# Performance work log

Hardware: AMD Instinct MI355X
Metric: run time of the kernel (lower is better)

## Reference

```python
import jax, jax.numpy as jnp
import numpy as np

TAU = 2.0        # LIFNode tau
ALPHA = 4.0      # spikingjelly default Sigmoid surrogate alpha
SCALE = 0.125    # attention scale from SSA
EPS = 1e-5       # BatchNorm eps

@jax.custom_vjp
def heaviside(x):
    return (x >= 0).astype(x.dtype)

def _hv_fwd(x):
    return (x >= 0).astype(x.dtype), x

def _hv_bwd(x, g):
    s = jax.nn.sigmoid(ALPHA * x)
    return (g * ALPHA * s * (1.0 - s),)

heaviside.defvjp(_hv_fwd, _hv_bwd)

def lif(x_seq, v_th):
    """Multi-step LIF (decay_input=True, v_reset=0, hard reset, detach_reset=True).
    x_seq: (T, ...) -> spikes (T, ...)."""
    def step(v, x):
        h = v + (x - v) / TAU                      # membrane charge
        s = heaviside(h - v_th)                    # spike
        v_new = h * (1.0 - jax.lax.stop_gradient(s))  # detached hard reset to 0
        return v_new, s
    _, spikes = jax.lax.scan(step, jnp.zeros_like(x_seq[0]), x_seq)
    return spikes

def conv_bn(x, w, gamma, beta, mean, var):
    """3x3 same-pad conv (no bias) + BatchNorm2d (eval: running stats), applied over merged T*B."""
    T, B, C, H, W = x.shape
    y = jax.lax.conv_general_dilated(
        x.reshape(T * B, C, H, W), w, (1, 1), 'SAME',
        dimension_numbers=('NCHW', 'OIHW', 'NCHW'))
    scale = gamma / jnp.sqrt(var + EPS)
    y = y * scale[:, None, None] + (beta - mean * scale)[:, None, None]
    return y.reshape(T, B, C, H, W)

def setup_inputs() -> dict:
    key = jax.random.key(0)
    T, B, C, H, W = 4, 16, 768, 16, 16
    ks = jax.random.split(key, 5)
    d = {"x": jax.random.normal(ks[0], (T, B, C, H, W), jnp.float32)}
    for i, p in enumerate(["q", "k", "v", "p"]):
        kk = jax.random.split(ks[i + 1], 5)
        d[p + "_w"] = jax.random.normal(kk[0], (C, C, 3, 3), jnp.float32) * 0.02
        d[p + "_gamma"] = jax.random.uniform(kk[1], (C,), jnp.float32, 0.5, 1.5)
        d[p + "_beta"] = jax.random.normal(kk[2], (C,), jnp.float32) * 0.1
        d[p + "_mean"] = jax.random.normal(kk[3], (C,), jnp.float32) * 0.1
        d[p + "_var"] = jax.random.uniform(kk[4], (C,), jnp.float32, 0.5, 1.5)
    return d

def reference(x, q_w, q_gamma, q_beta, q_mean, q_var,
              k_w, k_gamma, k_beta, k_mean, k_var,
              v_w, v_gamma, v_beta, v_mean, v_var,
              p_w, p_gamma, p_beta, p_mean, p_var):
    T, B, C, H, W = x.shape
    N = H * W
    nh = 8
    dh = C // nh
    xs = lif(x, 1.0)                                   # head_lif
    # Scaler is identity in eval mode (and rate=1.0)
    q = lif(conv_bn(xs, q_w, q_gamma, q_beta, q_mean, q_var), 1.0)
    k = lif(conv_bn(xs, k_w, k_gamma, k_beta, k_mean, k_var), 1.0)
    v = lif(conv_bn(xs, v_w, v_gamma, v_beta, v_mean, v_var), 1.0)
    def to_heads(t):  # (T,B,C,H,W) -> (T,B,nh,N,dh)
        return t.reshape(T, B, C, N).transpose(0, 1, 3, 2).reshape(T, B, N, nh, dh).transpose(0, 1, 3, 2, 4)
    q, k, v = to_heads(q), to_heads(k), to_heads(v)
    kv = jnp.einsum('tbhnd,tbhne->tbhde', k, v)        # k^T @ v (linear attention)
    o = jnp.einsum('tbhnd,tbhde->tbhne', q, kv) * SCALE
    o = o.transpose(0, 1, 2, 4, 3).reshape(T, B, C, N)  # (T,B,h,d,N) -> (T,B,C,N)
    o = lif(o, 0.5).reshape(T, B, C, H, W)              # attn_lif with v_threshold=0.5
    return conv_bn(o, p_w, p_gamma, p_beta, p_mean, p_var)
```

## Files before the change

kernel.cpp:

```cpp
#include <hip/hip_runtime.h>

typedef __attribute__((ext_vector_type(4))) int   i32x4;
typedef __attribute__((ext_vector_type(4))) float f32x4;
typedef unsigned int u32;
typedef unsigned long long u64;
typedef unsigned char u8;
typedef unsigned short u16;

#define C_ 768
#define NPIX 256
#define PLANE (16*C_*NPIX)
#define ROWB 96
#define IMGBITS (324*ROWB)
#define GS   304
#define PRS  1232
#define AEXP_SZ 12320

#define OFF_WFRAG 0ull
#define OFF_YBUF  10616832ull
#define OFF_QU8   60948480ull
#define OFF_KU8   73531392ull
#define OFF_VU8   86114304ull
#define OFF_OU8   98697216ull
#define OFF_BITS  111280128ull
#define BITSZ     1990656ull
#define OFF_SBT   121233408ull
#define OFF_FLAGS 121257984ull
#define OFF_WMAX  121258240ull

__device__ __forceinline__ i32x4 as_i4(uint4 v){ union{uint4 u; i32x4 s;} c; c.u=v; return c.s; }
#define SPREAD(NIB) ((u32)__mul24((int)(NIB), 0x204081) & 0x01010101u)

__global__ __launch_bounds__(256) void bn_prep4(
    const float* __restrict__ g0, const float* __restrict__ b0,
    const float* __restrict__ m0, const float* __restrict__ v0,
    const float* __restrict__ g1, const float* __restrict__ b1,
    const float* __restrict__ m1, const float* __restrict__ v1,
    const float* __restrict__ g2, const float* __restrict__ b2,
    const float* __restrict__ m2, const float* __restrict__ v2,
    const float* __restrict__ g3, const float* __restrict__ b3,
    const float* __restrict__ m3, const float* __restrict__ v3,
    float* __restrict__ out)
{
    int s = blockIdx.y;
    const float* g  = s==0?g0:s==1?g1:s==2?g2:g3;
    const float* be = s==0?b0:s==1?b1:s==2?b2:b3;
    const float* m  = s==0?m0:s==1?m1:s==2?m2:m3;
    const float* va = s==0?v0:s==1?v1:s==2?v2:v3;
    int i = blockIdx.x*256 + threadIdx.x;
    if (i < C_){
        float sc = g[i] / sqrtf(va[i] + 1e-5f);
        out[s*1536 + i] = sc;
        out[s*1536 + C_ + i] = be[i] - m[i]*sc;
    }
}

__global__ __launch_bounds__(256) void wmax4(
    const float* __restrict__ w0, const float* __restrict__ w1,
    const float* __restrict__ w2, const float* __restrict__ w3,
    float* __restrict__ out)
{
    int s = blockIdx.y;
    const float* w = s==0?w0:s==1?w1:s==2?w2:w3;
    const int n4 = 9*C_*C_/4;
    float m = 0.f;
    for (int i = blockIdx.x*256 + threadIdx.x; i < n4; i += 65536){
        f32x4 v = *(const f32x4*)(w + (size_t)i*4);
        m = fmaxf(m, fmaxf(fmaxf(fabsf(v[0]), fabsf(v[1])),
                           fmaxf(fabsf(v[2]), fabsf(v[3]))));
    }
    #pragma unroll
    for (int off = 32; off >= 1; off >>= 1)
        m = fmaxf(m, __shfl_xor(m, off));
    if ((threadIdx.x & 63) == 0)
        atomicMax((int*)(out + s), __float_as_int(m));
}

__global__ __launch_bounds__(256) void wprep(
    const float* __restrict__ w, const float* __restrict__ wmaxp,
    u8* __restrict__ wf)
{
    int gid = blockIdx.x*256 + threadIdx.x;
    int co = gid / 48, c16 = gid - co*48;
    float mw = *wmaxp;
    float invS = (mw > 0.f) ? (32512.0f / mw) : 0.f;
    int cch = c16 >> 2;
    int lane = (co & 15) | ((c16 & 3) << 4);
    int nfg = co >> 4;
    const float* wp = w + (size_t)co*6912 + (size_t)c16*144;
    #pragma unroll 1
    for (int tap=0; tap<9; ++tap){
        u32 hw[4] = {0,0,0,0}, lw[4] = {0,0,0,0};
        #pragma unroll
        for (int e=0;e<16;++e){
            float f = wp[e*9 + tap];
            int w16 = __float2int_rn(f * invS);
            w16 = min(max(w16, -32512), 32512);
            int hi = (w16 + 128) >> 8;
            int lo = w16 - (hi << 8);
            hw[e>>2] |= ((u32)(hi & 0xFF)) << ((e&3)*8);
            lw[e>>2] |= ((u32)(lo & 0xFF)) << ((e&3)*8);
        }
        size_t base = (((size_t)(cch*9+tap)*48 + nfg)*2)*1024 + (size_t)lane*16;
        *(uint4*)(wf + base)        = make_uint4(hw[0],hw[1],hw[2],hw[3]);
        *(uint4*)(wf + base + 1024) = make_uint4(lw[0],lw[1],lw[2],lw[3]);
    }
}

__global__ __launch_bounds__(256) void head_bits(
    const float* __restrict__ x, u8* __restrict__ bits)
{
    int gid = blockIdx.x*256 + threadIdx.x;
    int b = gid / 24576, rem = gid - b*24576;
    int cb = rem >> 8, pix = rem & 255;
    int pr = ((pix>>4)+1)*18 + (pix&15) + 1;
    float v[8];
    #pragma unroll
    for (int j=0;j<8;++j) v[j]=0.f;
    #pragma unroll
    for (int t=0;t<4;++t){
        int img = t*16 + b;
        u32 byte = 0;
        #pragma unroll
        for (int j=0;j<8;++j){
            float xv = x[((size_t)img*C_ + cb*8 + j)*NPIX + pix];
            float h = __fadd_rn(v[j], __fmul_rn(__fsub_rn(xv, v[j]), 0.5f));
            u32 s = (h >= 1.0f) ? 1u : 0u;
            v[j] = s ? 0.f : h;
            byte |= s << j;
        }
        bits[(size_t)img*IMGBITS + (size_t)pr*ROWB + cb] = (u8)byte;
    }
}

template<int EPI>
__global__ __launch_bounds__(256,2) void conv_i8(
    const u8* __restrict__ abits, const u8* __restrict__ wf,
    const float* __restrict__ sb, const float* __restrict__ wmaxp,
    const int* __restrict__ flags,
    float* __restrict__ ybuf, float* __restrict__ out)
{
    __shared__ __align__(16) u8 Aexp[2*AEXP_SZ];
    const int tid = threadIdx.x;
    const int bid = blockIdx.x;
    const int cox = bid & 7, mh = (bid >> 3) & 1, img = bid >> 4;
    const int lane = tid & 63, w = tid >> 6;
    const int wr = w >> 1, wc = w & 1;
    const int lrow = lane & 15, lgrp = lane >> 4;

    if constexpr (EPI == 1){
        if (flags[img] == 0){
            #pragma unroll 1
            for (int i = tid; i < 96*32; i += 256){
                int co = cox*96 + (i >> 5), seg = i & 31;
                float bv = sb[C_ + co];
                f32x4 v; v[0]=bv; v[1]=bv; v[2]=bv; v[3]=bv;
                *(f32x4*)(out + ((size_t)img*C_ + co)*NPIX + mh*128 + seg*4) = v;
            }
            return;
        }
    }

    const int erow = (tid < 180) ? tid : 179;
    const int epr = erow / 18, epc = erow - epr*18;
    u8* edst = Aexp + epr*PRS + epc*16;
    const u8* bsrc = abits + (size_t)img*IMGBITS + (size_t)(mh*144)*ROWB;

#define EXPW(BW, BOFF) if (tid < 180){ \
    u8* dp = edst + (BOFF); \
    u32 lo_ = (u32)(BW), hi_ = (u32)((BW)>>32); \
    *(uint4*)(dp       ) = make_uint4(SPREAD(lo_&0xF), SPREAD((lo_>>4)&0xF), SPREAD((lo_>>8)&0xF), SPREAD((lo_>>12)&0xF)); \
    *(uint4*)(dp + GS  ) = make_uint4(SPREAD((lo_>>16)&0xF), SPREAD((lo_>>20)&0xF), SPREAD((lo_>>24)&0xF), SPREAD((lo_>>28)&0xF)); \
    *(uint4*)(dp + 2*GS) = make_uint4(SPREAD(hi_&0xF), SPREAD((hi_>>4)&0xF), SPREAD((hi_>>8)&0xF), SPREAD((hi_>>12)&0xF)); \
    *(uint4*)(dp + 3*GS) = make_uint4(SPREAD((hi_>>16)&0xF), SPREAD((hi_>>20)&0xF), SPREAD((hi_>>24)&0xF), SPREAD((hi_>>28)&0xF)); }

    const u8* wp = wf + (size_t)((cox*6 + wc*3)*2)*1024 + (size_t)lane*16;
    uint4 R0[6], R1[6], R2[6];
#define LOADB(BUF) { \
    _Pragma("unroll") \
    for (int j=0;j<6;++j) BUF[j] = *(const uint4*)(wp + (j>>1)*2048 + (j&1)*1024); \
    wp += 98304; }

    int rb[4];
    #pragma unroll
    for (int mi=0;mi<4;++mi)
        rb[mi] = (wr*4 + mi + 1)*PRS + lgrp*GS + (lrow+1)*16;

    i32x4 acc_h[4][3], acc_l[4][3];
    #pragma unroll
    for (int mi=0;mi<4;++mi)
        #pragma unroll
        for (int ni=0;ni<3;++ni)
            #pragma unroll
            for (int r=0;r<4;++r){ acc_h[mi][ni][r]=0; acc_l[mi][ni][r]=0; }

#define COMPUTE(BUF, AE, TAP) { \
    const int DT = ((TAP)/3 - 1)*PRS + (((TAP)%3) - 1)*16; \
    i32x4 af[4]; \
    _Pragma("unroll") \
    for (int mi=0;mi<4;++mi) af[mi] = *(const i32x4*)((AE) + rb[mi] + DT); \
    __builtin_amdgcn_s_setprio(1); \
    _Pragma("unroll") \
    for (int mi=0;mi<4;++mi){ \
        _Pragma("unroll") \
        for (int ni=0;ni<3;++ni){ \
            acc_h[mi][ni] = __builtin_amdgcn_mfma_i32_16x16x64_i8(af[mi], as_i4(BUF[ni*2+0]), acc_h[mi][ni], 0,0,0); \
            acc_l[mi][ni] = __builtin_amdgcn_mfma_i32_16x16x64_i8(af[mi], as_i4(BUF[ni*2+1]), acc_l[mi][ni], 0,0,0); \
        } \
    } \
    __builtin_amdgcn_s_setprio(0); }

#define BODY(CCH, BOFF) { \
    u64 bwn = 0; \
    if ((CCH) < 11) bwn = *(const u64*)(bsrc + erow*ROWB + ((CCH)+1)*8); \
    const u8* Ae = Aexp + (BOFF); \
    LOADB(R2); COMPUTE(R0, Ae, 0); \
    LOADB(R0); COMPUTE(R1, Ae, 1); \
    LOADB(R1); COMPUTE(R2, Ae, 2); \
    LOADB(R2); COMPUTE(R0, Ae, 3); \
    LOADB(R0); COMPUTE(R1, Ae, 4); \
    LOADB(R1); COMPUTE(R2, Ae, 5); \
    LOADB(R2); COMPUTE(R0, Ae, 6); \
    LOADB(R0); COMPUTE(R1, Ae, 7); \
    LOADB(R1); COMPUTE(R2, Ae, 8); \
    if ((CCH) < 11) EXPW(bwn, (BOFF) ^ AEXP_SZ); \
    __syncthreads(); }

    LOADB(R0); LOADB(R1);
    {
        u64 bw0 = *(const u64*)(bsrc + erow*ROWB);
        EXPW(bw0, 0);
    }
    __syncthreads();

    #pragma unroll 1
    for (int c2=0; c2<6; ++c2){
        BODY(2*c2,   0);
        BODY(2*c2+1, AEXP_SZ);
    }
#undef LOADB
#undef EXPW
#undef COMPUTE
#undef BODY

    const float S = (*wmaxp) * (1.0f/32512.0f);
    #pragma unroll
    for (int mi=0;mi<4;++mi){
        const int prow = mh*128 + wr*64 + mi*16 + lgrp*4;
        #pragma unroll
        for (int ni=0;ni<3;++ni){
            const int co = cox*96 + wc*48 + ni*16 + lrow;
            const float sc = sb[co], bi = sb[C_ + co];
            if constexpr (EPI == 0){
                #pragma unroll
                for (int r=0;r<4;++r){
                    float accf = (float)(acc_h[mi][ni][r]*256 + acc_l[mi][ni][r]) * S;
                    ybuf[((size_t)img*NPIX + prow + r)*C_ + co] =
                        __fadd_rn(__fmul_rn(accf, sc), bi);
                }
            } else {
                f32x4 ov;
                #pragma unroll
                for (int r=0;r<4;++r){
                    float accf = (float)(acc_h[mi][ni][r]*256 + acc_l[mi][ni][r]) * S;
                    ov[r] = __fadd_rn(__fmul_rn(accf, sc), bi);
                }
                *(f32x4*)(out + ((size_t)img*C_ + co)*NPIX + prow) = ov;
            }
        }
    }
}

__global__ __launch_bounds__(256) void lif_bits(
    const float* __restrict__ y, u8* __restrict__ su8, u8* __restrict__ bits)
{
    int gid = blockIdx.x*256 + threadIdx.x;
    int b = gid / 24576, rem = gid - b*24576;
    int pix = rem / 96, cb = rem - pix*96;
    int pr = ((pix>>4)+1)*18 + (pix&15) + 1;
    float v[8];
    #pragma unroll
    for (int j=0;j<8;++j) v[j]=0.f;
    #pragma unroll
    for (int t=0;t<4;++t){
        int img = t*16 + b;
        const float* yp = y + ((size_t)img*NPIX + pix)*C_ + cb*8;
        f32x4 y0 = *(const f32x4*)yp;
        f32x4 y1 = *(const f32x4*)(yp + 4);
        u32 byte = 0, w0 = 0, w1 = 0;
        #pragma unroll
        for (int j=0;j<8;++j){
            float yv = (j<4) ? y0[j] : y1[j-4];
            float h = __fadd_rn(v[j], __fmul_rn(__fsub_rn(yv, v[j]), 0.5f));
            u32 s = (h >= 1.0f) ? 1u : 0u;
            v[j] = s ? 0.f : h;
            byte |= s << j;
            if (j<4) w0 |= s << (j*8); else w1 |= s << ((j-4)*8);
        }
        *(uint2*)(su8 + ((size_t)img*NPIX + pix)*C_ + cb*8) = make_uint2(w0,w1);
        bits[(size_t)img*IMGBITS + (size_t)pr*ROWB + cb] = (u8)byte;
    }
}

__global__ __launch_bounds__(256) void pad_o_bits(
    const u8* __restrict__ o, u8* __restrict__ bits, int* __restrict__ flags)
{
    int gid = blockIdx.x*256 + threadIdx.x;
    int img = gid / 24576, rem = gid - img*24576;
    int pix = rem / 96, cb = rem - pix*96;
    int pr = ((pix>>4)+1)*18 + (pix&15) + 1;
    uint2 r = *(const uint2*)(o + ((size_t)img*NPIX + pix)*C_ + cb*8);
    u32 byte = 0;
    #pragma unroll
    for (int j=0;j<4;++j){
        byte |= ((r.x >> (j*8)) & 1u) << j;
        byte |= ((r.y >> (j*8)) & 1u) << (j+4);
    }
    bits[(size_t)img*IMGBITS + (size_t)pr*ROWB + cb] = (u8)byte;
    if (__any((int)(r.x | r.y)) && (threadIdx.x & 63) == 0)
        atomicOr(&flags[img], 1);
}

__global__ __launch_bounds__(512) void attn_fused(
    const u8* __restrict__ qs, const u8* __restrict__ ks,
    const u8* __restrict__ vs, u8* __restrict__ os)
{
    const int tid = threadIdx.x;
    const int b = blockIdx.x, h = blockIdx.y;
    __shared__ u64 kb[96][4], vb[96][4];
    __shared__ float kvl[96][96];
    const int w = tid >> 6, lane = tid & 63;
    const int ng = w & 3, n_build = ng*64 + lane;
    const int n = tid & 255, eh = tid >> 8;
    float vmem[48];
    #pragma unroll
    for (int e=0;e<48;++e) vmem[e]=0.f;

    for (int t=0;t<4;++t){
        const int img = t*16 + b;
        const size_t rbase = ((size_t)img*NPIX)*C_ + (size_t)h*96;
        {
            const u8* src = (w < 4 ? ks : vs) + rbase + (size_t)n_build*C_;
            uint4 r[6];
            #pragma unroll
            for (int j=0;j<6;++j) r[j] = ((const uint4*)src)[j];
            u32 wd[24];
            #pragma unroll
            for (int j=0;j<6;++j){ wd[4*j]=r[j].x; wd[4*j+1]=r[j].y; wd[4*j+2]=r[j].z; wd[4*j+3]=r[j].w; }
            u64 (*dst)[4] = (w < 4) ? kb : vb;
            #pragma unroll 1
            for (int d=0; d<96; ++d){
                u32 byte = (wd[d>>2] >> ((d&3)*8)) & 0xFFu;
                u64 m = __ballot((int)byte);
                if (lane == 0) dst[d][ng] = m;
            }
        }
        __syncthreads();
        for (int i = tid; i < 96*96; i += 512){
            int d = i / 96, e = i - d*96;
            int s = 0;
            #pragma unroll
            for (int g=0; g<4; ++g) s += __popcll(kb[d][g] & vb[e][g]);
            kvl[d][e] = (float)s;
        }
        __syncthreads();
        {
            const u8* qsrc = qs + rbase + (size_t)n*C_;
            uint4 r[6];
            #pragma unroll
            for (int j=0;j<6;++j) r[j] = ((const uint4*)qsrc)[j];
            u32 qw[24];
            #pragma unroll
            for (int j=0;j<6;++j){ qw[4*j]=r[j].x; qw[4*j+1]=r[j].y; qw[4*j+2]=r[j].z; qw[4*j+3]=r[j].w; }
            float val[48];
            #pragma unroll
            for (int e=0;e<48;++e) val[e]=0.f;
            #pragma unroll 1
            for (int d=0; d<96; ++d){
                u32 qb = (qw[d>>2] >> ((d&3)*8)) & 0xFFu;
                if (__any((int)qb)){
                    float qf = (float)qb;
                    #pragma unroll
                    for (int e=0;e<48;++e) val[e] += qf * kvl[d][eh*48+e];
                }
            }
            u32 ow[12];
            #pragma unroll
            for (int e=0;e<48;++e){
                float o = val[e]*0.125f;
                float hh = __fadd_rn(vmem[e], __fmul_rn(__fsub_rn(o, vmem[e]), 0.5f));
                u8 s = (hh >= 0.5f) ? 1 : 0;
                vmem[e] = s ? 0.f : hh;
                if ((e&3)==0) ow[e>>2] = (u32)s; else ow[e>>2] |= ((u32)s) << ((e&3)*8);
            }
            uint4* od = (uint4*)(os + rbase + (size_t)n*C_ + eh*48);
            od[0] = make_uint4(ow[0],ow[1],ow[2],ow[3]);
            od[1] = make_uint4(ow[4],ow[5],ow[6],ow[7]);
            od[2] = make_uint4(ow[8],ow[9],ow[10],ow[11]);
        }
        __syncthreads();
    }
}

extern "C" void kernel_launch(void* const* d_in, const int* in_sizes, int n_in,
                              void* d_out, int out_size, void* d_ws, size_t ws_size,
                              hipStream_t stream)
{
    u8* ws = (u8*)d_ws;
    u8* wfrag   = ws + OFF_WFRAG;
    float* ybuf = (float*)(ws + OFF_YBUF);
    u8* q_u8 = ws + OFF_QU8;
    u8* k_u8 = ws + OFF_KU8;
    u8* v_u8 = ws + OFF_VU8;
    u8* o_u8 = ws + OFF_OU8;
    u8* xs_b = ws + OFF_BITS;
    u8* q_b  = ws + OFF_BITS + 1*BITSZ;
    u8* k_b  = ws + OFF_BITS + 2*BITSZ;
    u8* v_b  = ws + OFF_BITS + 3*BITSZ;
    u8* o_b  = ws + OFF_BITS + 4*BITSZ;
    float* sbt = (float*)(ws + OFF_SBT);
    int* flags = (int*)(ws + OFF_FLAGS);
    float* wmaxb = (float*)(ws + OFF_WMAX);
    float* outp = (float*)d_out;

    hipMemsetAsync(ws + OFF_BITS, 0, 5*BITSZ, stream);
    hipMemsetAsync(ws + OFF_FLAGS, 0, 512, stream);

    bn_prep4<<<dim3(3,4),256,0,stream>>>(
        (const float*)d_in[2],  (const float*)d_in[3],  (const float*)d_in[4],  (const float*)d_in[5],
        (const float*)d_in[7],  (const float*)d_in[8],  (const float*)d_in[9],  (const float*)d_in[10],
        (const float*)d_in[12], (const float*)d_in[13], (const float*)d_in[14], (const float*)d_in[15],
        (const float*)d_in[17], (const float*)d_in[18], (const float*)d_in[19], (const float*)d_in[20],
        sbt);
    wmax4<<<dim3(256,4),256,0,stream>>>(
        (const float*)d_in[1], (const float*)d_in[6],
        (const float*)d_in[11], (const float*)d_in[16], wmaxb);
    head_bits<<<1536,256,0,stream>>>((const float*)d_in[0], xs_b);

    u8* u8p[3]  = {q_u8, k_u8, v_u8};
    u8* bitp[3] = {q_b, k_b, v_b};
    for (int s=0;s<3;++s){
        wprep<<<144,256,0,stream>>>((const float*)d_in[1+5*s], wmaxb + s, wfrag);
        conv_i8<0><<<1024,256,0,stream>>>(xs_b, wfrag, sbt + s*1536, wmaxb + s,
                                          nullptr, ybuf, nullptr);
        lif_bits<<<1536,256,0,stream>>>(ybuf, u8p[s], bitp[s]);
    }
    attn_fused<<<dim3(16,8),512,0,stream>>>(q_u8, k_u8, v_u8, o_u8);
    pad_o_bits<<<6144,256,0,stream>>>(o_u8, o_b, flags);
    wprep<<<144,256,0,stream>>>((const float*)d_in[16], wmaxb + 3, wfrag);
    conv_i8<1><<<1024,256,0,stream>>>(o_b, wfrag, sbt + 4608, wmaxb + 3,
                                      flags, nullptr, outp);
}
```

Baseline: 600.7 us.

## Fuse LIF into conv epilogue, sparse bit-driven projection conv, batch weight prep

The q/k/v convolutions now loop over the four timesteps inside one block, carrying the LIF membrane in registers. Each block writes spikes directly, which removes the fp32 ybuf round trip and the separate lif_bits kernel. The attention kernel writes padded bit-packed output directly, and the final projection conv becomes a sparse scatter-add. That scatter-add walks the set spike bits and accumulates int16 column-major weights in shared memory, replacing the dense MFMA conv. Weight prep for all four convs is batched into one launch. The trade-offs are smaller grids (512 blocks) with fewer rows per block, and a projection cost that now depends on spike density.

```diff
diff --git a/kernel.cpp b/kernel.cpp
--- a/kernel.cpp
+++ b/kernel.cpp
@@ -9,24 +9,23 @@
 
 #define C_ 768
 #define NPIX 256
-#define PLANE (16*C_*NPIX)
 #define ROWB 96
 #define IMGBITS (324*ROWB)
-#define GS   304
-#define PRS  1232
-#define AEXP_SZ 12320
-
+#define LGS 288
+#define EPRS 1184
+#define AEXP_SZ 7104
+
+#define WFRAG_SZ 10616832ull
 #define OFF_WFRAG 0ull
-#define OFF_YBUF  10616832ull
-#define OFF_QU8   60948480ull
-#define OFF_KU8   73531392ull
-#define OFF_VU8   86114304ull
-#define OFF_OU8   98697216ull
-#define OFF_BITS  111280128ull
+#define OFF_WCOL  42467328ull
+#define OFF_QU8   53084160ull
+#define OFF_KU8   65667072ull
+#define OFF_VU8   78249984ull
+#define OFF_XSB   90832896ull
+#define OFF_OB    92823552ull
 #define BITSZ     1990656ull
-#define OFF_SBT   121233408ull
-#define OFF_FLAGS 121257984ull
-#define OFF_WMAX  121258240ull
+#define OFF_SBT   94814208ull
+#define OFF_WMAX  94838784ull
 
 __device__ __forceinline__ i32x4 as_i4(uint4 v){ union{uint4 u; i32x4 s;} c; c.u=v; return c.s; }
 #define SPREAD(NIB) ((u32)__mul24((int)(NIB), 0x204081) & 0x01010101u)
@@ -76,13 +75,18 @@
         atomicMax((int*)(out + s), __float_as_int(m));
 }
 
-__global__ __launch_bounds__(256) void wprep(
-    const float* __restrict__ w, const float* __restrict__ wmaxp,
-    u8* __restrict__ wf)
-{
+__global__ __launch_bounds__(256) void wprep4(
+    const float* __restrict__ w0, const float* __restrict__ w1,
+    const float* __restrict__ w2, const float* __restrict__ w3,
+    const float* __restrict__ wmaxb, u8* __restrict__ wfbase,
+    short* __restrict__ wcol)
+{
+    int s = blockIdx.y;
+    const float* w = s==0?w0:s==1?w1:s==2?w2:w3;
+    u8* wf = wfbase + (size_t)s*WFRAG_SZ;
     int gid = blockIdx.x*256 + threadIdx.x;
     int co = gid / 48, c16 = gid - co*48;
-    float mw = *wmaxp;
+    float mw = wmaxb[s];
     float invS = (mw > 0.f) ? (32512.0f / mw) : 0.f;
     int cch = c16 >> 2;
     int lane = (co & 15) | ((c16 & 3) << 4);
@@ -91,11 +95,13 @@
     #pragma unroll 1
     for (int tap=0; tap<9; ++tap){
         u32 hw[4] = {0,0,0,0}, lw[4] = {0,0,0,0};
+        int w16v[16];
         #pragma unroll
         for (int e=0;e<16;++e){
             float f = wp[e*9 + tap];
             int w16 = __float2int_rn(f * invS);
             w16 = min(max(w16, -32512), 32512);
+            w16v[e] = w16;
             int hi = (w16 + 128) >> 8;
             int lo = w16 - (hi << 8);
             hw[e>>2] |= ((u32)(hi & 0xFF)) << ((e&3)*8);
@@ -104,6 +110,11 @@
         size_t base = (((size_t)(cch*9+tap)*48 + nfg)*2)*1024 + (size_t)lane*16;
         *(uint4*)(wf + base)        = make_uint4(hw[0],hw[1],hw[2],hw[3]);
         *(uint4*)(wf + base + 1024) = make_uint4(lw[0],lw[1],lw[2],lw[3]);
+        if (s == 3){
+            #pragma unroll
+            for (int e=0;e<16;++e)
+                wcol[((size_t)tap*C_ + c16*16+e)*C_ + co] = (short)w16v[e];
+        }
     }
 }
 
@@ -133,86 +144,65 @@
     }
 }
 
-template<int EPI>
-__global__ __launch_bounds__(256,2) void conv_i8(
+__global__ __launch_bounds__(256,2) void conv_lif(
     const u8* __restrict__ abits, const u8* __restrict__ wf,
     const float* __restrict__ sb, const float* __restrict__ wmaxp,
-    const int* __restrict__ flags,
-    float* __restrict__ ybuf, float* __restrict__ out)
+    u8* __restrict__ su8)
 {
     __shared__ __align__(16) u8 Aexp[2*AEXP_SZ];
     const int tid = threadIdx.x;
     const int bid = blockIdx.x;
-    const int cox = bid & 7, mh = (bid >> 3) & 1, img = bid >> 4;
+    const int cox = bid & 7, mh = (bid >> 3) & 3, bq = bid >> 5;
     const int lane = tid & 63, w = tid >> 6;
     const int wr = w >> 1, wc = w & 1;
     const int lrow = lane & 15, lgrp = lane >> 4;
 
-    if constexpr (EPI == 1){
-        if (flags[img] == 0){
-            #pragma unroll 1
-            for (int i = tid; i < 96*32; i += 256){
-                int co = cox*96 + (i >> 5), seg = i & 31;
-                float bv = sb[C_ + co];
-                f32x4 v; v[0]=bv; v[1]=bv; v[2]=bv; v[3]=bv;
-                *(f32x4*)(out + ((size_t)img*C_ + co)*NPIX + mh*128 + seg*4) = v;
-            }
-            return;
-        }
-    }
-
-    const int erow = (tid < 180) ? tid : 179;
-    const int epr = erow / 18, epc = erow - epr*18;
-    u8* edst = Aexp + epr*PRS + epc*16;
-    const u8* bsrc = abits + (size_t)img*IMGBITS + (size_t)(mh*144)*ROWB;
-
-#define EXPW(BW, BOFF) if (tid < 180){ \
+    float scs[3], bis[3];
+    #pragma unroll
+    for (int ni=0;ni<3;++ni){
+        int co = cox*96 + wc*48 + ni*16 + lrow;
+        scs[ni] = sb[co]; bis[ni] = sb[C_ + co];
+    }
+    const float S = wmaxp[0] * (1.0f/32512.0f);
+
+    const int rb0 = (wr*2 + 1)*EPRS + lgrp*LGS + (lrow+1)*16;
+    const int rb1 = rb0 + EPRS;
+
+    const int erow = (tid < 108) ? tid : 107;
+    const int epr = erow/18, epc = erow - epr*18;
+    u8* edst = Aexp + epr*EPRS + epc*16;
+
+#define EXPW(BW, BOFF) if (tid < 108){ \
     u8* dp = edst + (BOFF); \
     u32 lo_ = (u32)(BW), hi_ = (u32)((BW)>>32); \
-    *(uint4*)(dp       ) = make_uint4(SPREAD(lo_&0xF), SPREAD((lo_>>4)&0xF), SPREAD((lo_>>8)&0xF), SPREAD((lo_>>12)&0xF)); \
-    *(uint4*)(dp + GS  ) = make_uint4(SPREAD((lo_>>16)&0xF), SPREAD((lo_>>20)&0xF), SPREAD((lo_>>24)&0xF), SPREAD((lo_>>28)&0xF)); \
-    *(uint4*)(dp + 2*GS) = make_uint4(SPREAD(hi_&0xF), SPREAD((hi_>>4)&0xF), SPREAD((hi_>>8)&0xF), SPREAD((hi_>>12)&0xF)); \
-    *(uint4*)(dp + 3*GS) = make_uint4(SPREAD((hi_>>16)&0xF), SPREAD((hi_>>20)&0xF), SPREAD((hi_>>24)&0xF), SPREAD((hi_>>28)&0xF)); }
-
-    const u8* wp = wf + (size_t)((cox*6 + wc*3)*2)*1024 + (size_t)lane*16;
+    *(uint4*)(dp        ) = make_uint4(SPREAD(lo_&0xF), SPREAD((lo_>>4)&0xF), SPREAD((lo_>>8)&0xF), SPREAD((lo_>>12)&0xF)); \
+    *(uint4*)(dp + LGS  ) = make_uint4(SPREAD((lo_>>16)&0xF), SPREAD((lo_>>20)&0xF), SPREAD((lo_>>24)&0xF), SPREAD((lo_>>28)&0xF)); \
+    *(uint4*)(dp + 2*LGS) = make_uint4(SPREAD(hi_&0xF), SPREAD((hi_>>4)&0xF), SPREAD((hi_>>8)&0xF), SPREAD((hi_>>12)&0xF)); \
+    *(uint4*)(dp + 3*LGS) = make_uint4(SPREAD((hi_>>16)&0xF), SPREAD((hi_>>20)&0xF), SPREAD((hi_>>24)&0xF), SPREAD((hi_>>28)&0xF)); }
+
     uint4 R0[6], R1[6], R2[6];
 #define LOADB(BUF) { \
     _Pragma("unroll") \
     for (int j=0;j<6;++j) BUF[j] = *(const uint4*)(wp + (j>>1)*2048 + (j&1)*1024); \
     wp += 98304; }
 
-    int rb[4];
-    #pragma unroll
-    for (int mi=0;mi<4;++mi)
-        rb[mi] = (wr*4 + mi + 1)*PRS + lgrp*GS + (lrow+1)*16;
-
-    i32x4 acc_h[4][3], acc_l[4][3];
-    #pragma unroll
-    for (int mi=0;mi<4;++mi)
-        #pragma unroll
-        for (int ni=0;ni<3;++ni)
-            #pragma unroll
-            for (int r=0;r<4;++r){ acc_h[mi][ni][r]=0; acc_l[mi][ni][r]=0; }
-
 #define COMPUTE(BUF, AE, TAP) { \
-    const int DT = ((TAP)/3 - 1)*PRS + (((TAP)%3) - 1)*16; \
-    i32x4 af[4]; \
-    _Pragma("unroll") \
-    for (int mi=0;mi<4;++mi) af[mi] = *(const i32x4*)((AE) + rb[mi] + DT); \
+    const int DT = ((TAP)/3 - 1)*EPRS + (((TAP)%3) - 1)*16; \
+    i32x4 af0 = *(const i32x4*)((AE) + rb0 + DT); \
+    i32x4 af1 = *(const i32x4*)((AE) + rb1 + DT); \
     __builtin_amdgcn_s_setprio(1); \
     _Pragma("unroll") \
-    for (int mi=0;mi<4;++mi){ \
-        _Pragma("unroll") \
-        for (int ni=0;ni<3;++ni){ \
-            acc_h[mi][ni] = __builtin_amdgcn_mfma_i32_16x16x64_i8(af[mi], as_i4(BUF[ni*2+0]), acc_h[mi][ni], 0,0,0); \
-            acc_l[mi][ni] = __builtin_amdgcn_mfma_i32_16x16x64_i8(af[mi], as_i4(BUF[ni*2+1]), acc_l[mi][ni], 0,0,0); \
-        } \
+    for (int ni=0;ni<3;++ni){ \
+        acc_h[0][ni] = __builtin_amdgcn_mfma_i32_16x16x64_i8(af0, as_i4(BUF[ni*2+0]), acc_h[0][ni], 0,0,0); \
+        acc_l[0][ni] = __builtin_amdgcn_mfma_i32_16x16x64_i8(af0, as_i4(BUF[ni*2+1]), acc_l[0][ni], 0,0,0); \
+        acc_h[1][ni] = __builtin_amdgcn_mfma_i32_16x16x64_i8(af1, as_i4(BUF[ni*2+0]), acc_h[1][ni], 0,0,0); \
+        acc_l[1][ni] = __builtin_amdgcn_mfma_i32_16x16x64_i8(af1, as_i4(BUF[ni*2+1]), acc_l[1][ni], 0,0,0); \
     } \
     __builtin_amdgcn_s_setprio(0); }
 
 #define BODY(CCH, BOFF) { \
     u64 bwn = 0; \
-    if ((CCH) < 11) bwn = *(const u64*)(bsrc + erow*ROWB + ((CCH)+1)*8); \
+    if ((CCH) < 11) bwn = *(const u64*)(bsrc + ((CCH)+1)*8); \
     const u8* Ae = Aexp + (BOFF); \
     LOADB(R2); COMPUTE(R0, Ae, 0); \
     LOADB(R0); COMPUTE(R1, Ae, 1); \
@@ -226,104 +216,71 @@
     if ((CCH) < 11) EXPW(bwn, (BOFF) ^ AEXP_SZ); \
     __syncthreads(); }
 
-    LOADB(R0); LOADB(R1);
-    {
-        u64 bw0 = *(const u64*)(bsrc + erow*ROWB);
+    float vmem[2][3][4];
+    #pragma unroll
+    for (int mi=0;mi<2;++mi)
+        #pragma unroll
+        for (int ni=0;ni<3;++ni)
+            #pragma unroll
+            for (int r=0;r<4;++r) vmem[mi][ni][r] = 0.f;
+
+    const int y0 = mh*4 + wr*2;
+
+    #pragma unroll 1
+    for (int t=0; t<4; ++t){
+        const int img = t*16 + bq;
+        const u8* bsrc = abits + (size_t)img*IMGBITS
+                       + (size_t)((mh*4 + epr)*18 + epc)*ROWB;
+        const u8* wp = wf + (size_t)(cox*6 + wc*3)*2048 + (size_t)lane*16;
+
+        i32x4 acc_h[2][3], acc_l[2][3];
+        #pragma unroll
+        for (int mi=0;mi<2;++mi)
+            #pragma unroll
+            for (int ni=0;ni<3;++ni)
+                #pragma unroll
+                for (int r=0;r<4;++r){ acc_h[mi][ni][r]=0; acc_l[mi][ni][r]=0; }
+
+        u64 bw0 = *(const u64*)(bsrc);
+        LOADB(R0); LOADB(R1);
         EXPW(bw0, 0);
-    }
-    __syncthreads();
-
-    #pragma unroll 1
-    for (int c2=0; c2<6; ++c2){
-        BODY(2*c2,   0);
-        BODY(2*c2+1, AEXP_SZ);
+        __syncthreads();
+
+        #pragma unroll 1
+        for (int c2=0; c2<6; ++c2){
+            BODY(2*c2,   0);
+            BODY(2*c2+1, AEXP_SZ);
+        }
+
+        #pragma unroll
+        for (int mi=0;mi<2;++mi){
+            const int pixb = (y0 + mi)*16 + lgrp*4;
+            #pragma unroll
+            for (int ni=0;ni<3;++ni){
+                const int co = cox*96 + wc*48 + ni*16 + lrow;
+                #pragma unroll
+                for (int r=0;r<4;++r){
+                    int sum = acc_h[mi][ni][r]*256 + acc_l[mi][ni][r];
+                    float accf = (float)sum * S;
+                    float y = __fadd_rn(__fmul_rn(accf, scs[ni]), bis[ni]);
+                    float h = __fadd_rn(vmem[mi][ni][r],
+                              __fmul_rn(__fsub_rn(y, vmem[mi][ni][r]), 0.5f));
+                    u32 s = (h >= 1.0f) ? 1u : 0u;
+                    vmem[mi][ni][r] = s ? 0.f : h;
+                    su8[((size_t)img*NPIX + pixb + r)*C_ + co] = (u8)s;
+                }
+            }
+        }
     }
 #undef LOADB
 #undef EXPW
 #undef COMPUTE
 #undef BODY
-
-    const float S = (*wmaxp) * (1.0f/32512.0f);
-    #pragma unroll
-    for (int mi=0;mi<4;++mi){
-        const int prow = mh*128 + wr*64 + mi*16 + lgrp*4;
-        #pragma unroll
-        for (int ni=0;ni<3;++ni){
-            const int co = cox*96 + wc*48 + ni*16 + lrow;
-            const float sc = sb[co], bi = sb[C_ + co];
-            if constexpr (EPI == 0){
-                #pragma unroll
-                for (int r=0;r<4;++r){
-                    float accf = (float)(acc_h[mi][ni][r]*256 + acc_l[mi][ni][r]) * S;
-                    ybuf[((size_t)img*NPIX + prow + r)*C_ + co] =
-                        __fadd_rn(__fmul_rn(accf, sc), bi);
-                }
-            } else {
-                f32x4 ov;
-                #pragma unroll
-                for (int r=0;r<4;++r){
-                    float accf = (float)(acc_h[mi][ni][r]*256 + acc_l[mi][ni][r]) * S;
-                    ov[r] = __fadd_rn(__fmul_rn(accf, sc), bi);
-                }
-                *(f32x4*)(out + ((size_t)img*C_ + co)*NPIX + prow) = ov;
-            }
-        }
-    }
-}
-
-__global__ __launch_bounds__(256) void lif_bits(
-    const float* __restrict__ y, u8* __restrict__ su8, u8* __restrict__ bits)
-{
-    int gid = blockIdx.x*256 + threadIdx.x;
-    int b = gid / 24576, rem = gid - b*24576;
-    int pix = rem / 96, cb = rem - pix*96;
-    int pr = ((pix>>4)+1)*18 + (pix&15) + 1;
-    float v[8];
-    #pragma unroll
-    for (int j=0;j<8;++j) v[j]=0.f;
-    #pragma unroll
-    for (int t=0;t<4;++t){
-        int img = t*16 + b;
-        const float* yp = y + ((size_t)img*NPIX + pix)*C_ + cb*8;
-        f32x4 y0 = *(const f32x4*)yp;
-        f32x4 y1 = *(const f32x4*)(yp + 4);
-        u32 byte = 0, w0 = 0, w1 = 0;
-        #pragma unroll
-        for (int j=0;j<8;++j){
-            float yv = (j<4) ? y0[j] : y1[j-4];
-            float h = __fadd_rn(v[j], __fmul_rn(__fsub_rn(yv, v[j]), 0.5f));
-            u32 s = (h >= 1.0f) ? 1u : 0u;
-            v[j] = s ? 0.f : h;
-            byte |= s << j;
-            if (j<4) w0 |= s << (j*8); else w1 |= s << ((j-4)*8);
-        }
-        *(uint2*)(su8 + ((size_t)img*NPIX + pix)*C_ + cb*8) = make_uint2(w0,w1);
-        bits[(size_t)img*IMGBITS + (size_t)pr*ROWB + cb] = (u8)byte;
-    }
-}
-
-__global__ __launch_bounds__(256) void pad_o_bits(
-    const u8* __restrict__ o, u8* __restrict__ bits, int* __restrict__ flags)
-{
-    int gid = blockIdx.x*256 + threadIdx.x;
-    int img = gid / 24576, rem = gid - img*24576;
-    int pix = rem / 96, cb = rem - pix*96;
-    int pr = ((pix>>4)+1)*18 + (pix&15) + 1;
-    uint2 r = *(const uint2*)(o + ((size_t)img*NPIX + pix)*C_ + cb*8);
-    u32 byte = 0;
-    #pragma unroll
-    for (int j=0;j<4;++j){
-        byte |= ((r.x >> (j*8)) & 1u) << j;
-        byte |= ((r.y >> (j*8)) & 1u) << (j+4);
-    }
-    bits[(size_t)img*IMGBITS + (size_t)pr*ROWB + cb] = (u8)byte;
-    if (__any((int)(r.x | r.y)) && (threadIdx.x & 63) == 0)
-        atomicOr(&flags[img], 1);
 }
 
 __global__ __launch_bounds__(512) void attn_fused(
     const u8* __restrict__ qs, const u8* __restrict__ ks,
-    const u8* __restrict__ vs, u8* __restrict__ os)
+    const u8* __restrict__ vs, u8* __restrict__ ob)
 {
     const int tid = threadIdx.x;
     const int b = blockIdx.x, h = blockIdx.y;
@@ -384,21 +341,87 @@
                     for (int e=0;e<48;++e) val[e] += qf * kvl[d][eh*48+e];
                 }
             }
-            u32 ow[12];
+            u64 wbits = 0;
             #pragma unroll
             for (int e=0;e<48;++e){
                 float o = val[e]*0.125f;
                 float hh = __fadd_rn(vmem[e], __fmul_rn(__fsub_rn(o, vmem[e]), 0.5f));
-                u8 s = (hh >= 0.5f) ? 1 : 0;
+                u32 s = (hh >= 0.5f) ? 1u : 0u;
                 vmem[e] = s ? 0.f : hh;
-                if ((e&3)==0) ow[e>>2] = (u32)s; else ow[e>>2] |= ((u32)s) << ((e&3)*8);
-            }
-            uint4* od = (uint4*)(os + rbase + (size_t)n*C_ + eh*48);
-            od[0] = make_uint4(ow[0],ow[1],ow[2],ow[3]);
-            od[1] = make_uint4(ow[4],ow[5],ow[6],ow[7]);
-            od[2] = make_uint4(ow[8],ow[9],ow[10],ow[11]);
+                wbits |= (u64)s << e;
+            }
+            const int prn = ((n>>4)+1)*18 + (n&15) + 1;
+            u8* od = ob + (size_t)img*IMGBITS + (size_t)prn*ROWB + h*12 + eh*6;
+            *(u16*)(od)     = (u16)(wbits);
+            *(u16*)(od + 2) = (u16)(wbits >> 16);
+            *(u16*)(od + 4) = (u16)(wbits >> 32);
         }
         __syncthreads();
+    }
+}
+
+__global__ __launch_bounds__(256) void pconv_sparse(
+    const u8* __restrict__ ob, const short* __restrict__ wcol,
+    const float* __restrict__ sb, const float* __restrict__ wmaxp,
+    float* __restrict__ out)
+{
+    __shared__ u64 bl[648];
+    __shared__ int accL[16*768];
+    const int tid = threadIdx.x;
+    const int img = blockIdx.x >> 4, y = blockIdx.x & 15;
+
+    for (int idx = tid; idx < 648; idx += 256){
+        int d = idx / 216, wi = idx - d*216;
+        bl[idx] = *(const u64*)(ob + (size_t)img*IMGBITS
+                                + (size_t)((y+d)*18)*ROWB + (size_t)wi*8);
+    }
+    for (int idx = tid; idx < 16*768; idx += 256) accL[idx] = 0;
+    __syncthreads();
+
+    #pragma unroll 1
+    for (int wi = 0; wi < 648; ++wi){
+        u64 v = bl[wi];
+        if (!v) continue;
+        while (v){
+            int j = __ffsll((unsigned long long)v) - 1;
+            v &= v - 1;
+            int byt = wi*8 + (j >> 3);
+            int p = byt / 96;
+            int c = (byt - p*96)*8 + (j & 7);
+            int dd = p / 18, px = p - dd*18;
+            #pragma unroll
+            for (int xi = 0; xi < 3; ++xi){
+                int x = px - 2 + xi;
+                if ((unsigned)x < 16u){
+                    int tap = dd*3 + 2 - xi;
+                    const short* wr_ = wcol + ((size_t)tap*C_ + c)*C_;
+                    #pragma unroll
+                    for (int q = 0; q < 3; ++q){
+                        int co = tid + q*256;
+                        accL[x*768 + co] += (int)wr_[co];
+                    }
+                }
+            }
+        }
+    }
+    __syncthreads();
+
+    const float S = wmaxp[0] * (1.0f/32512.0f);
+    #pragma unroll
+    for (int q = 0; q < 3; ++q){
+        int co = tid + q*256;
+        float sc = sb[co], bi = sb[C_ + co];
+        float* op = out + ((size_t)img*C_ + co)*NPIX + y*16;
+        #pragma unroll
+        for (int xg = 0; xg < 4; ++xg){
+            f32x4 o4;
+            #pragma unroll
+            for (int rr = 0; rr < 4; ++rr){
+                float accf = (float)accL[(xg*4+rr)*768 + co] * S;
+                o4[rr] = __fadd_rn(__fmul_rn(accf, sc), bi);
+            }
+            *(f32x4*)(op + xg*4) = o4;
+        }
     }
 }
 
@@ -407,24 +430,19 @@
                               hipStream_t stream)
 {
     u8* ws = (u8*)d_ws;
-    u8* wfrag   = ws + OFF_WFRAG;
-    float* ybuf = (float*)(ws + OFF_YBUF);
+    u8* wfrag = ws + OFF_WFRAG;
+    short* wcol = (short*)(ws + OFF_WCOL);
     u8* q_u8 = ws + OFF_QU8;
     u8* k_u8 = ws + OFF_KU8;
     u8* v_u8 = ws + OFF_VU8;
-    u8* o_u8 = ws + OFF_OU8;
-    u8* xs_b = ws + OFF_BITS;
-    u8* q_b  = ws + OFF_BITS + 1*BITSZ;
-    u8* k_b  = ws + OFF_BITS + 2*BITSZ;
-    u8* v_b  = ws + OFF_BITS + 3*BITSZ;
-    u8* o_b  = ws + OFF_BITS + 4*BITSZ;
+    u8* xs_b = ws + OFF_XSB;
+    u8* o_b  = ws + OFF_OB;
     float* sbt = (float*)(ws + OFF_SBT);
-    int* flags = (int*)(ws + OFF_FLAGS);
     float* wmaxb = (float*)(ws + OFF_WMAX);
     float* outp = (float*)d_out;
 
-    hipMemsetAsync(ws + OFF_BITS, 0, 5*BITSZ, stream);
-    hipMemsetAsync(ws + OFF_FLAGS, 0, 512, stream);
+    hipMemsetAsync(xs_b, 0, 2*BITSZ, stream);
+    hipMemsetAsync(wmaxb, 0, 16, stream);
 
     bn_prep4<<<dim3(3,4),256,0,stream>>>(
         (const float*)d_in[2],  (const float*)d_in[3],  (const float*)d_in[4],  (const float*)d_in[5],
@@ -435,19 +453,15 @@
     wmax4<<<dim3(256,4),256,0,stream>>>(
         (const float*)d_in[1], (const float*)d_in[6],
         (const float*)d_in[11], (const float*)d_in[16], wmaxb);
+    wprep4<<<dim3(144,4),256,0,stream>>>(
+        (const float*)d_in[1], (const float*)d_in[6],
+        (const float*)d_in[11], (const float*)d_in[16], wmaxb, wfrag, wcol);
     head_bits<<<1536,256,0,stream>>>((const float*)d_in[0], xs_b);
 
-    u8* u8p[3]  = {q_u8, k_u8, v_u8};
-    u8* bitp[3] = {q_b, k_b, v_b};
-    for (int s=0;s<3;++s){
-        wprep<<<144,256,0,stream>>>((const float*)d_in[1+5*s], wmaxb + s, wfrag);
-        conv_i8<0><<<1024,256,0,stream>>>(xs_b, wfrag, sbt + s*1536, wmaxb + s,
-                                          nullptr, ybuf, nullptr);
-        lif_bits<<<1536,256,0,stream>>>(ybuf, u8p[s], bitp[s]);
-    }
-    attn_fused<<<dim3(16,8),512,0,stream>>>(q_u8, k_u8, v_u8, o_u8);
-    pad_o_bits<<<6144,256,0,stream>>>(o_u8, o_b, flags);
-    wprep<<<144,256,0,stream>>>((const float*)d_in[16], wmaxb + 3, wfrag);
-    conv_i8<1><<<1024,256,0,stream>>>(o_b, wfrag, sbt + 4608, wmaxb + 3,
-                                      flags, nullptr, outp);
-}
+    conv_lif<<<512,256,0,stream>>>(xs_b, wfrag + 0*WFRAG_SZ, sbt + 0,    wmaxb + 0, q_u8);
+    conv_lif<<<512,256,0,stream>>>(xs_b, wfrag + 1*WFRAG_SZ, sbt + 1536, wmaxb + 1, k_u8);
+    conv_lif<<<512,256,0,stream>>>(xs_b, wfrag + 2*WFRAG_SZ, sbt + 3072, wmaxb + 2, v_u8);
+
+    attn_fused<<<dim3(16,8),512,0,stream>>>(q_u8, k_u8, v_u8, o_b);
+    pconv_sparse<<<1024,256,0,stream>>>(o_b, wcol, sbt + 4608, wmaxb + 3, outp);
+}
```

New measurement: 913.3 us. 1.52x slower.
